# Performance work log

Measured on AMD Instinct MI355X. Metric: run time of the kernel, lower is better.

The kernel has to match this reference:

```python
import math
import jax, jax.numpy as jnp
import numpy as np

H, C, PQ, PV = 8, 256, 8, 12   # no_heads, c_hidden, no_qk_points, no_v_points
INF, EPS = 1e5, 1e-8

def quat_to_rot(q):
    w, x, y, z = q[..., 0], q[..., 1], q[..., 2], q[..., 3]
    r = jnp.stack([
        1 - 2*(y*y + z*z), 2*(x*y - w*z),     2*(x*z + w*y),
        2*(x*y + w*z),     1 - 2*(x*x + z*z), 2*(y*z - w*x),
        2*(x*z - w*y),     2*(y*z + w*x),     1 - 2*(x*x + y*y),
    ], axis=-1)
    return r.reshape(q.shape[:-1] + (3, 3))

def setup_inputs() -> dict:
    key = jax.random.key(0)
    ks = jax.random.split(key, 16)
    B, N, CS, CZ = 1, 512, 384, 128
    s = jax.random.normal(ks[0], (B, N, CS), jnp.float32)
    z = jax.random.normal(ks[1], (B, N, N, CZ), jnp.float32) * 0.1
    quat = jax.random.normal(ks[2], (B, N, 4), jnp.float32)
    quat = quat / jnp.linalg.norm(quat, axis=-1, keepdims=True)
    rot = quat_to_rot(quat)                       # [B,N,3,3] valid rotations
    trans = jax.random.normal(ks[3], (B, N, 3), jnp.float32) * 10.0
    mask = jnp.ones((B, N), jnp.float32)
    g = lambda k, sh: jax.random.normal(k, sh, jnp.float32) * 0.02
    params = dict(
        wq=g(ks[4], (CS, H*C)), bq=jnp.zeros((H*C,), jnp.float32),
        wkv=g(ks[5], (CS, 2*H*C)), bkv=jnp.zeros((2*H*C,), jnp.float32),
        wqp=g(ks[6], (CS, H*PQ*3)), bqp=jnp.zeros((H*PQ*3,), jnp.float32),
        wkvp=g(ks[7], (CS, H*(PQ+PV)*3)), bkvp=jnp.zeros((H*(PQ+PV)*3,), jnp.float32),
        wb=g(ks[8], (CZ, H)), bb=jnp.zeros((H,), jnp.float32),
        wz=g(ks[9], (CZ, CZ//4)), bz=jnp.zeros((CZ//4,), jnp.float32),
        head_weights=jnp.full((H,), 0.541324854612918, jnp.float32),  # softplus^-1(1)
        wo=g(ks[10], (H*(C + 4*PV + CZ//4), CS)), bo=jnp.zeros((CS,), jnp.float32),
    )
    return dict(s=s, z=z, rot=rot, trans=trans, mask=mask, **params)

def reference(s, z, rot, trans, mask, wq, bq, wkv, bkv, wqp, bqp, wkvp, bkvp, wb, bb, wz, bz, head_weights, wo, bo):
    B, N, CS = s.shape
    q = (s @ wq + bq).reshape(B, N, H, C)
    kv = (s @ wkv + bkv).reshape(B, N, H, 2 * C)
    k, v = kv[..., :C], kv[..., C:]

    def split_pts(x):  # torch split-into-3 + stack(-1): [B,N,3*M] -> [B,N,M,3]
        return jnp.moveaxis(x.reshape(B, N, 3, -1), -2, -1)

    def apply_rigid(p):  # global frame: R @ p + t
        return jnp.einsum('bnij,bnpj->bnpi', rot, p) + trans[:, :, None, :]

    q_pts = apply_rigid(split_pts(s @ wqp + bqp)).reshape(B, N, H, PQ, 3)
    kv_pts = apply_rigid(split_pts(s @ wkvp + bkvp)).reshape(B, N, H, PQ + PV, 3)
    k_pts, v_pts = kv_pts[..., :PQ, :], kv_pts[..., PQ:, :]

    b_bias = z @ wb + bb                                  # [B,Ni,Nj,H]
    a = jnp.einsum('bihc,bjhc->bhij', q, k) * math.sqrt(1.0 / (3 * C))
    a = a + math.sqrt(1.0 / 3) * jnp.moveaxis(b_bias, -1, 1)

    disp = q_pts[:, :, None] - k_pts[:, None]             # [B,Ni,Nj,H,PQ,3]
    pt_att = jnp.sum(disp * disp, axis=-1)                # [B,Ni,Nj,H,PQ]
    hw = jax.nn.softplus(head_weights) * math.sqrt(1.0 / (3 * (PQ * 9.0 / 2)))
    pt_att = -0.5 * jnp.sum(pt_att * hw[None, None, None, :, None], axis=-1)  # [B,Ni,Nj,H]

    sq_mask = INF * (mask[:, :, None] * mask[:, None, :] - 1.0)
    a = a + jnp.moveaxis(pt_att, -1, 1) + sq_mask[:, None]
    a = jax.nn.softmax(a, axis=-1)                        # [B,H,Ni,Nj]

    o = jnp.einsum('bhij,bjhc->bihc', a, v).reshape(B, N, H * C)

    o_pt = jnp.einsum('bhij,bjhpd->bihpd', a, v_pts)      # [B,N,H,PV,3] global
    o_pt = jnp.einsum('bnji,bnhpj->bnhpi', rot, o_pt - trans[:, :, None, None, :])  # invert_apply
    o_pt_norm = jnp.sqrt(jnp.sum(o_pt * o_pt, axis=-1) + EPS).reshape(B, N, H * PV)
    o_pt_flat = o_pt.reshape(B, N, H * PV, 3)

    pair_z = z @ wz + bz                                  # [B,Ni,Nj,CZ//4]
    o_pair = jnp.einsum('bhij,bijd->bihd', a, pair_z).reshape(B, N, -1)

    feats = jnp.concatenate(
        [o, o_pt_flat[..., 0], o_pt_flat[..., 1], o_pt_flat[..., 2], o_pt_norm, o_pair], axis=-1)
    return feats @ wo + bo
```

## Files before the change

kernel.cpp:

```cpp
#include <hip/hip_runtime.h>


#define OFF_QBH    0
#define OFF_KBH    524288
#define OFF_VB     1048576
#define OFF_QPRAW  2097152
#define OFF_KVPRAW 2195456
#define OFF_BBIAS  2785280
#define OFF_PAIRZT 3833856
#define OFF_ATTNH  8028160
#define OFF_FEATSB 9076736
#define OFF_WCAT   9764864
#define OFF_WTALL  9767936
#define OFF_VPT    11082752
#define OFF_WOT    11803648
#define OFF_QPTH   12319744
#define OFF_QPTL   12385280
#define OFF_KPTH   12450816
#define OFF_KPTL   12516352
#define OFF_QP2    12581888
#define OFF_KP2    12585984
#define OFF_SBF    12590080

typedef __attribute__((ext_vector_type(8))) short short8;
typedef __attribute__((ext_vector_type(4))) float f32x4;

__device__ __forceinline__ unsigned short f2bf(float f) {
  union { float f; unsigned u; } v; v.f = f;
  unsigned u = v.u;
  unsigned r = (u + 0x7fffu + ((u >> 16) & 1u)) >> 16;
  return (unsigned short)r;
}
__device__ __forceinline__ float bf2f(unsigned short h) {
  union { unsigned u; float f; } v; v.u = ((unsigned)h) << 16; return v.f;
}
__device__ __forceinline__ short8 pack8(float4 a, float4 b) {
  short8 r;
  r[0] = (short)f2bf(a.x); r[1] = (short)f2bf(a.y);
  r[2] = (short)f2bf(a.z); r[3] = (short)f2bf(a.w);
  r[4] = (short)f2bf(b.x); r[5] = (short)f2bf(b.y);
  r[6] = (short)f2bf(b.z); r[7] = (short)f2bf(b.w);
  return r;
}
__device__ __forceinline__ void gl_lds16(const float* g, float* l) {
  __builtin_amdgcn_global_load_lds(
      (const __attribute__((address_space(1))) unsigned int*)(g),
      (__attribute__((address_space(3))) unsigned int*)(l), 16, 0, 0);
}

__global__ __launch_bounds__(256) void prep_all(
    const float* __restrict__ wq, const float* __restrict__ wkv,
    const float* __restrict__ wqp, const float* __restrict__ wkvp,
    const float* __restrict__ wo, const float* __restrict__ wb,
    const float* __restrict__ wz, const float* __restrict__ s,
    unsigned short* __restrict__ wTall, unsigned short* __restrict__ woT,
    unsigned short* __restrict__ wT, unsigned short* __restrict__ sbf) {
  __shared__ float tile[64][65];
  const int b = blockIdx.x, t = threadIdx.x;
  if (b < 642) {
    const int ntile = b % 107, kt = b / 107;
    const float* src; int Nsrc, nloc0;
    const int ng0 = ntile * 64;
    if (ntile < 32)      { src = wq;   Nsrc = 2048; nloc0 = ng0; }
    else if (ntile < 96) { src = wkv;  Nsrc = 4096; nloc0 = ng0 - 2048; }
    else if (ntile < 99) { src = wqp;  Nsrc = 192;  nloc0 = ng0 - 6144; }
    else                 { src = wkvp; Nsrc = 480;  nloc0 = ng0 - 6336; }
    const int r = t >> 2, cs = (t & 3) * 16;
#pragma unroll
    for (int i = 0; i < 16; i += 4) {
      int n = nloc0 + cs + i;
      float4 v;
      if (n + 3 < Nsrc) v = *(const float4*)(src + (size_t)(kt * 64 + r) * Nsrc + n);
      else {
        v.x = (n + 0 < Nsrc) ? src[(size_t)(kt * 64 + r) * Nsrc + n + 0] : 0.f;
        v.y = (n + 1 < Nsrc) ? src[(size_t)(kt * 64 + r) * Nsrc + n + 1] : 0.f;
        v.z = (n + 2 < Nsrc) ? src[(size_t)(kt * 64 + r) * Nsrc + n + 2] : 0.f;
        v.w = (n + 3 < Nsrc) ? src[(size_t)(kt * 64 + r) * Nsrc + n + 3] : 0.f;
      }
      tile[r][cs + i + 0] = v.x; tile[r][cs + i + 1] = v.y;
      tile[r][cs + i + 2] = v.z; tile[r][cs + i + 3] = v.w;
    }
    __syncthreads();
    const int nr = t >> 2, ks = (t & 3) * 16;
    unsigned short ov[16];
#pragma unroll
    for (int i = 0; i < 16; i++) ov[i] = f2bf(tile[ks + i][nr]);
    unsigned short* dst = wTall + (size_t)(ng0 + nr) * 384 + kt * 64 + ks;
    *(uint4*)(dst) = *(const uint4*)&ov[0];
    *(uint4*)(dst + 8) = *(const uint4*)&ov[8];
  } else if (b < 894) {
    const int idx = b - 642;
    const int kt = idx % 42, ntile = idx / 42;
    const int r = t >> 2, cs = (t & 3) * 16;
#pragma unroll
    for (int i = 0; i < 16; i += 4) {
      float4 v = *(const float4*)(wo + (size_t)(kt * 64 + r) * 384 + ntile * 64 + cs + i);
      tile[r][cs + i + 0] = v.x; tile[r][cs + i + 1] = v.y;
      tile[r][cs + i + 2] = v.z; tile[r][cs + i + 3] = v.w;
    }
    __syncthreads();
    const int nr = t >> 2, ks = (t & 3) * 16;
    unsigned short ov[16];
#pragma unroll
    for (int i = 0; i < 16; i++) ov[i] = f2bf(tile[ks + i][nr]);
    unsigned short* dst = woT + (size_t)(ntile * 64 + nr) * 2688 + kt * 64 + ks;
    *(uint4*)(dst) = *(const uint4*)&ov[0];
    *(uint4*)(dst + 8) = *(const uint4*)&ov[8];
  } else if (b < 918) {
    const int l = (b - 894) * 256 + t;
    if (l < 6144) {
      int n = l >> 7, k = l & 127;
      float v = (n < 8) ? wb[k * 8 + n] * 0.5773502691896258f
                        : (n < 40 ? wz[k * 32 + (n - 8)] : 0.f);
      wT[l] = f2bf(v);
    }
  } else {
    const int gid = (b - 918) * 256 + t;
    const int off = gid * 8;
    float4 a0 = *(const float4*)(s + off);
    float4 a1 = *(const float4*)(s + off + 4);
    *(short8*)(sbf + off) = pack8(a0, a1);
  }
}

__global__ __launch_bounds__(256) void mega1(
    const float* __restrict__ z, const unsigned short* __restrict__ wT,
    const float* __restrict__ bb, const float* __restrict__ bz,
    unsigned short* __restrict__ bbias_tb, unsigned short* __restrict__ pairzT,
    const unsigned short* __restrict__ sbf, const unsigned short* __restrict__ wTall,
    const float* __restrict__ bq, const float* __restrict__ bkv,
    const float* __restrict__ bqp, const float* __restrict__ bkvp,
    unsigned short* __restrict__ qbh, unsigned short* __restrict__ kbh,
    float* __restrict__ vb, float* __restrict__ qpraw, float* __restrict__ kvpraw) {
  const int lane = threadIdx.x & 63, wv = threadIdx.x >> 6;
  const int quad = lane >> 4, m = lane & 15;
  if (blockIdx.x < 256) {
    __shared__ __align__(16) float zt[2][64][128];
    __shared__ __align__(16) unsigned short lb[4][8][16];
    __shared__ __align__(16) unsigned short lp[4][32][16];
    short8 bfw[3][4];
#pragma unroll
    for (int nt = 0; nt < 3; nt++)
#pragma unroll
      for (int s = 0; s < 4; s++)
        bfw[nt][s] = *(const short8*)(wT + (size_t)(nt * 16 + m) * 128 + s * 32 + quad * 8);
    float bias[3];
#pragma unroll
    for (int nt = 0; nt < 3; nt++) {
      int c = nt * 16 + m;
      bias[nt] = (c < 8) ? 0.5773502691896258f * bb[c] : (c < 40 ? bz[c - 8] : 0.f);
    }
    const int lrow = lane >> 5, lcol = (lane & 31) * 4;
    {
      const int Tg0 = blockIdx.x * 16;
#pragma unroll
      for (int i2 = 0; i2 < 8; i2++) {
        const int k = wv * 8 + i2;
        gl_lds16(z + (size_t)(Tg0 * 64 + 2 * k + lrow) * 128 + lcol, &zt[0][2 * k][0]);
      }
    }
    __syncthreads();
    for (int T = 0; T < 16; T++) {
      const int buf = T & 1;
      const int Tg = blockIdx.x * 16 + T;
      if (T < 15) {
#pragma unroll
        for (int i2 = 0; i2 < 8; i2++) {
          const int k = wv * 8 + i2;
          gl_lds16(z + (size_t)((Tg + 1) * 64 + 2 * k + lrow) * 128 + lcol,
                   &zt[buf ^ 1][2 * k][0]);
        }
      }
      f32x4 acc[3];
#pragma unroll
      for (int nt = 0; nt < 3; nt++) acc[nt] = (f32x4){0.f, 0.f, 0.f, 0.f};
#pragma unroll
      for (int s = 0; s < 4; s++) {
        const float* zr = &zt[buf][wv * 16 + m][s * 32 + quad * 8];
        float4 a0 = *(const float4*)(zr);
        float4 a1 = *(const float4*)(zr + 4);
        short8 af = pack8(a0, a1);
#pragma unroll
        for (int nt = 0; nt < 3; nt++)
          acc[nt] = __builtin_amdgcn_mfma_f32_16x16x32_bf16(af, bfw[nt][s], acc[nt], 0, 0, 0);
      }
#pragma unroll
      for (int nt = 0; nt < 3; nt++) {
        const int c = nt * 16 + m;
#pragma unroll
        for (int r = 0; r < 4; r++) {
          const float v = acc[nt][r] + bias[nt];
          const int jl = quad * 4 + r;
          if (c < 8)       lb[wv][c][jl] = f2bf(v);
          else if (c < 40) lp[wv][c - 8][jl] = f2bf(v);
        }
      }
      const int row0 = Tg * 64 + wv * 16;
      const int i = row0 >> 9, j0 = row0 & 511;
      if (lane < 16) {
        int c = lane >> 1, half = lane & 1;
        uint4 val = *(const uint4*)&lb[wv][c][half * 8];
        *(uint4*)(bbias_tb + (size_t)c * 262144 + row0 + half * 8) = val;
      }
      {
        int d = lane >> 1, half = lane & 1;
        uint4 val = *(const uint4*)&lp[wv][d][half * 8];
        *(uint4*)(pairzT + ((size_t)i * 32 + d) * 512 + j0 + half * 8) = val;
      }
      __syncthreads();
    }
  } else {
    const int b2 = blockIdx.x - 256;
    const int bx = b2 % 107, row0 = (b2 / 107) * 64;
    const int n0 = bx * 64;
    const unsigned short* srow = sbf + (size_t)(row0 + wv * 16 + m) * 384;
    f32x4 acc[4];
#pragma unroll
    for (int nt = 0; nt < 4; nt++) acc[nt] = (f32x4){0.f, 0.f, 0.f, 0.f};
#pragma unroll
    for (int ksx = 0; ksx < 12; ksx++) {
      const int c0 = ksx * 32 + quad * 8;
      short8 af = *(const short8*)(srow + c0);
#pragma unroll
      for (int nt = 0; nt < 4; nt++) {
        short8 bfw2 = *(const short8*)(wTall + (size_t)(n0 + nt * 16 + m) * 384 + c0);
        acc[nt] = __builtin_amdgcn_mfma_f32_16x16x32_bf16(af, bfw2, acc[nt], 0, 0, 0);
      }
    }
    const int rbase = row0 + wv * 16 + quad * 4;
#pragma unroll
    for (int nt = 0; nt < 4; nt++) {
      const int col = n0 + nt * 16 + m;
      if (n0 < 2048) {
        const float bias = bq[col];
#pragma unroll
        for (int r = 0; r < 4; r++)
          qbh[(size_t)(rbase + r) * 2048 + col] = f2bf(acc[nt][r] + bias);
      } else if (n0 < 6144) {
        const int ckv = col - 2048;
        const float bias = bkv[ckv];
        const int hh = ckv >> 9, c = ckv & 511;
        if (c < 256) {
#pragma unroll
          for (int r = 0; r < 4; r++)
            kbh[(size_t)(rbase + r) * 2048 + hh * 256 + c] = f2bf(acc[nt][r] + bias);
        } else {
#pragma unroll
          for (int r = 0; r < 4; r++)
            vb[(size_t)(rbase + r) * 2048 + hh * 256 + (c - 256)] = acc[nt][r] + bias;
        }
      } else if (n0 < 6336) {
        const int cq = col - 6144;
        const float bias = bqp[cq];
#pragma unroll
        for (int r = 0; r < 4; r++)
          qpraw[(size_t)(rbase + r) * 192 + cq] = acc[nt][r] + bias;
      } else {
        const int ck = col - 6336;
        if (ck < 480) {
          const float bias = bkvp[ck];
#pragma unroll
          for (int r = 0; r < 4; r++)
            kvpraw[(size_t)(rbase + r) * 480 + ck] = acc[nt][r] + bias;
        }
      }
    }
  }
}

__global__ __launch_bounds__(256) void mega2(
    const float* __restrict__ vb, const float* __restrict__ qpraw,
    const float* __restrict__ kvpraw, const float* __restrict__ rot,
    const float* __restrict__ trans, unsigned short* __restrict__ vptT,
    unsigned short* __restrict__ qptH, unsigned short* __restrict__ qptL,
    unsigned short* __restrict__ kptH, unsigned short* __restrict__ kptL,
    float* __restrict__ qp2g, float* __restrict__ kp2g) {
  __shared__ float tile[64][65];
  const int b = blockIdx.x, t = threadIdx.x;
  if (b < 320) {
    const int jt = b & 7, h = (b >> 3) & 7, part = b >> 6;
    const int j0 = jt * 64;
    if (part < 4) {
      const int c0 = part * 64;
      const int r = t >> 2, cs = (t & 3) * 16;
#pragma unroll
      for (int ii = 0; ii < 16; ii += 4) {
        float4 v = *(const float4*)(vb + (size_t)(j0 + r) * 2048 + h * 256 + c0 + cs + ii);
        tile[r][cs + ii + 0] = v.x; tile[r][cs + ii + 1] = v.y;
        tile[r][cs + ii + 2] = v.z; tile[r][cs + ii + 3] = v.w;
      }
      __syncthreads();
      const int cl = t >> 2, js = (t & 3) * 16;
      unsigned short ov[16];
#pragma unroll
      for (int x = 0; x < 16; x++) ov[x] = f2bf(tile[js + x][cl]);
      unsigned short* dst = vptT + ((size_t)h * 352 + c0 + cl) * 512 + j0 + js;
      *(uint4*)dst = *(const uint4*)&ov[0];
      *(uint4*)(dst + 8) = *(const uint4*)&ov[8];
    } else {
      float (*lds)[37] = (float(*)[37])&tile[0][0];
      for (int l = t; l < 64 * 36; l += 256) {
        int jl = l / 36, w = l % 36;
        int p = w / 3, d = w % 3;
        const int n = j0 + jl;
        const int pidx = h * 20 + 8 + p;
        const float* kr = kvpraw + (size_t)n * 480;
        float px = kr[pidx], py = kr[160 + pidx], pz = kr[320 + pidx];
        const float* R = rot + n * 9;
        lds[jl][w] = R[d * 3 + 0] * px + R[d * 3 + 1] * py + R[d * 3 + 2] * pz + trans[n * 3 + d];
      }
      __syncthreads();
#pragma unroll
      for (int step = 0; step < 3; step++) {
        int chunk = t + 256 * step;
        int row = chunk >> 3, js = (chunk & 7) * 8;
        unsigned short ov[8];
#pragma unroll
        for (int x = 0; x < 8; x++) {
          int w = (row < 48) ? row : row - 48;
          float f = (w < 36) ? lds[js + x][w] : 0.f;
          unsigned short hi = f2bf(f);
          ov[x] = (row < 48) ? hi : f2bf(f - bf2f(hi));
        }
        *(uint4*)(vptT + ((size_t)h * 352 + 256 + row) * 512 + j0 + js) = *(const uint4*)&ov[0];
      }
    }
  } else {
    const int idx = b - 320;
    const int row = (idx & 1) * 256 + t;
    const int h = idx >> 1;
    const float* R  = rot + row * 9;
    const float* tr = trans + row * 3;
    {
      const float* qr = qpraw + (size_t)row * 192;
      unsigned short hi[32], lo[32]; float s2 = 0.f;
#pragma unroll
      for (int p = 0; p < 8; p++) {
        const int pidx = h * 8 + p;
        float px = qr[pidx], py = qr[64 + pidx], pz = qr[128 + pidx];
        float X = R[0] * px + R[1] * py + R[2] * pz + tr[0];
        float Y = R[3] * px + R[4] * py + R[5] * pz + tr[1];
        float Z = R[6] * px + R[7] * py + R[8] * pz + tr[2];
        hi[p * 3 + 0] = f2bf(X); lo[p * 3 + 0] = f2bf(X - bf2f(hi[p * 3 + 0]));
        hi[p * 3 + 1] = f2bf(Y); lo[p * 3 + 1] = f2bf(Y - bf2f(hi[p * 3 + 1]));
        hi[p * 3 + 2] = f2bf(Z); lo[p * 3 + 2] = f2bf(Z - bf2f(hi[p * 3 + 2]));
        s2 += X * X + Y * Y + Z * Z;
      }
#pragma unroll
      for (int w = 24; w < 32; w++) { hi[w] = 0; lo[w] = 0; }
      unsigned short* dh = qptH + ((size_t)h * 512 + row) * 32;
      unsigned short* dl = qptL + ((size_t)h * 512 + row) * 32;
#pragma unroll
      for (int g = 0; g < 4; g++) {
        *(uint4*)(dh + g * 8) = *(const uint4*)&hi[g * 8];
        *(uint4*)(dl + g * 8) = *(const uint4*)&lo[g * 8];
      }
      qp2g[h * 512 + row] = s2;
    }
    {
      const float* kr = kvpraw + (size_t)row * 480;
      unsigned short hi[32], lo[32]; float s2 = 0.f;
#pragma unroll
      for (int p = 0; p < 8; p++) {
        const int pidx = h * 20 + p;
        float px = kr[pidx], py = kr[160 + pidx], pz = kr[320 + pidx];
        float X = R[0] * px + R[1] * py + R[2] * pz + tr[0];
        float Y = R[3] * px + R[4] * py + R[5] * pz + tr[1];
        float Z = R[6] * px + R[7] * py + R[8] * pz + tr[2];
        hi[p * 3 + 0] = f2bf(X); lo[p * 3 + 0] = f2bf(X - bf2f(hi[p * 3 + 0]));
        hi[p * 3 + 1] = f2bf(Y); lo[p * 3 + 1] = f2bf(Y - bf2f(hi[p * 3 + 1]));
        hi[p * 3 + 2] = f2bf(Z); lo[p * 3 + 2] = f2bf(Z - bf2f(hi[p * 3 + 2]));
        s2 += X * X + Y * Y + Z * Z;
      }
#pragma unroll
      for (int w = 24; w < 32; w++) { hi[w] = 0; lo[w] = 0; }
      unsigned short* dh = kptH + ((size_t)h * 512 + row) * 32;
      unsigned short* dl = kptL + ((size_t)h * 512 + row) * 32;
#pragma unroll
      for (int g = 0; g < 4; g++) {
        *(uint4*)(dh + g * 8) = *(const uint4*)&hi[g * 8];
        *(uint4*)(dl + g * 8) = *(const uint4*)&lo[g * 8];
      }
      kp2g[h * 512 + row] = s2;
    }
  }
}

__global__ __launch_bounds__(512) void logits_fused(
    const unsigned short* __restrict__ qbh, const unsigned short* __restrict__ kbh,
    const unsigned short* __restrict__ qptH, const unsigned short* __restrict__ qptL,
    const unsigned short* __restrict__ kptH, const unsigned short* __restrict__ kptL,
    const float* __restrict__ qp2g, const float* __restrict__ kp2g,
    const unsigned short* __restrict__ bbias_tb, const float* __restrict__ mask,
    const float* __restrict__ hwp, const unsigned short* __restrict__ vptT,
    const float* __restrict__ rot, const float* __restrict__ trans,
    unsigned short* __restrict__ attnh, unsigned short* __restrict__ featsb) {
  const int bx = blockIdx.x;
  const int h = bx & 7, it = bx >> 3;
  const int i0 = it * 16;
  __shared__ __align__(16) unsigned short sth[8][16][72], stl[8][16][72];
  __shared__ float redm[16][8], reds[16][8];
  __shared__ float lds_h[16][48], lds_l[16][48];
  const int t = threadIdx.x;
  const int lane = t & 63, wv = t >> 6;
  const int quad = lane >> 4, m = lane & 15;
  const int jw0 = wv * 64;

  f32x4 acc[4];
#pragma unroll
  for (int nt = 0; nt < 4; nt++) acc[nt] = (f32x4){0.f, 0.f, 0.f, 0.f};
  const unsigned short* qrow = qbh + (size_t)(i0 + m) * 2048 + h * 256;
#pragma unroll
  for (int s = 0; s < 8; s++) {
    short8 af = *(const short8*)(qrow + s * 32 + quad * 8);
#pragma unroll
    for (int nt = 0; nt < 4; nt++) {
      short8 bfr = *(const short8*)(kbh + (size_t)(jw0 + nt * 16 + m) * 2048 + h * 256 + s * 32 + quad * 8);
      acc[nt] = __builtin_amdgcn_mfma_f32_16x16x32_bf16(af, bfr, acc[nt], 0, 0, 0);
    }
  }

  short8 aqh = *(const short8*)(qptH + ((size_t)h * 512 + i0 + m) * 32 + quad * 8);
  short8 aql = *(const short8*)(qptL + ((size_t)h * 512 + i0 + m) * 32 + quad * 8);
  f32x4 accp[4];
#pragma unroll
  for (int nt = 0; nt < 4; nt++) {
    const size_t krow = ((size_t)h * 512 + jw0 + nt * 16 + m) * 32 + quad * 8;
    short8 bkh = *(const short8*)(kptH + krow);
    short8 bkl = *(const short8*)(kptL + krow);
    f32x4 p = (f32x4){0.f, 0.f, 0.f, 0.f};
    p = __builtin_amdgcn_mfma_f32_16x16x32_bf16(aqh, bkh, p, 0, 0, 0);
    p = __builtin_amdgcn_mfma_f32_16x16x32_bf16(aqh, bkl, p, 0, 0, 0);
    p = __builtin_amdgcn_mfma_f32_16x16x32_bf16(aql, bkh, p, 0, 0, 0);
    accp[nt] = p;
  }

  const float c1 = 0.03608439182435161f;
  const float hw = log1pf(expf(hwp[h])) * 0.09622504486493764f;
  float qp2v[4];
#pragma unroll
  for (int r = 0; r < 4; r++) qp2v[r] = qp2g[h * 512 + i0 + quad * 4 + r];
  float lg[4][4];
  float rmax[4] = {-1e30f, -1e30f, -1e30f, -1e30f};
#pragma unroll
  for (int nt = 0; nt < 4; nt++) {
    const int j = jw0 + nt * 16 + m;
    const float kp2v = kp2g[h * 512 + j];
    const float mj = mask[j];
#pragma unroll
    for (int r = 0; r < 4; r++) {
      const int il = quad * 4 + r;
      const float pt = qp2v[r] + kp2v - 2.f * accp[nt][r];
      float v = c1 * acc[nt][r]
              + bf2f(bbias_tb[(size_t)h * 262144 + (size_t)(i0 + il) * 512 + j])
              - 0.5f * hw * pt
              + 100000.f * (mask[i0 + il] * mj - 1.f);
      lg[nt][r] = v;
      rmax[r] = fmaxf(rmax[r], v);
    }
  }
#pragma unroll
  for (int r = 0; r < 4; r++) {
#pragma unroll
    for (int off = 1; off < 16; off <<= 1) rmax[r] = fmaxf(rmax[r], __shfl_xor(rmax[r], off));
  }
  if (m == 0) {
#pragma unroll
    for (int r = 0; r < 4; r++) redm[quad * 4 + r][wv] = rmax[r];
  }
  __syncthreads();
  float rowm[4], rsum[4];
#pragma unroll
  for (int r = 0; r < 4; r++) {
    const int il = quad * 4 + r;
    float m0 = fmaxf(fmaxf(redm[il][0], redm[il][1]), fmaxf(redm[il][2], redm[il][3]));
    float m1 = fmaxf(fmaxf(redm[il][4], redm[il][5]), fmaxf(redm[il][6], redm[il][7]));
    rowm[r] = fmaxf(m0, m1);
    rsum[r] = 0.f;
  }
#pragma unroll
  for (int nt = 0; nt < 4; nt++)
#pragma unroll
    for (int r = 0; r < 4; r++) {
      float e = __expf(lg[nt][r] - rowm[r]);
      lg[nt][r] = e;
      rsum[r] += e;
    }
#pragma unroll
  for (int r = 0; r < 4; r++) {
#pragma unroll
    for (int off = 1; off < 16; off <<= 1) rsum[r] += __shfl_xor(rsum[r], off);
  }
  if (m == 0) {
#pragma unroll
    for (int r = 0; r < 4; r++) reds[quad * 4 + r][wv] = rsum[r];
  }
  __syncthreads();
  float inv[4];
#pragma unroll
  for (int r = 0; r < 4; r++) {
    const int il = quad * 4 + r;
    float s0 = (reds[il][0] + reds[il][1]) + (reds[il][2] + reds[il][3]);
    float s1 = (reds[il][4] + reds[il][5]) + (reds[il][6] + reds[il][7]);
    inv[r] = 1.f / (s0 + s1);
  }
#pragma unroll
  for (int nt = 0; nt < 4; nt++)
#pragma unroll
    for (int r = 0; r < 4; r++) {
      const int il = quad * 4 + r;
      float a = lg[nt][r] * inv[r];
      unsigned short hi = f2bf(a);
      sth[wv][il][nt * 16 + m] = hi;
      stl[wv][il][nt * 16 + m] = f2bf(a - bf2f(hi));
    }
  __syncthreads();
#pragma unroll
  for (int step = 0; step < 2; step++) {
    const int idx = lane + 64 * step;
    const int il = idx >> 3, seg = idx & 7;
    uint4 vh = *(const uint4*)&sth[wv][il][seg * 8];
    *(uint4*)(attnh + ((size_t)h * 512 + i0 + il) * 512 + jw0 + seg * 8) = vh;
  }

  const int nt0 = (wv < 6) ? wv * 3 : 18 + (wv - 6) * 2;
  const int ncnt = (wv < 6) ? 3 : 2;
  f32x4 vacc[3];
#pragma unroll
  for (int k = 0; k < 3; k++) vacc[k] = (f32x4){0.f, 0.f, 0.f, 0.f};
  const unsigned short* vbase = vptT + (size_t)h * 352 * 512;
#pragma unroll
  for (int s = 0; s < 16; s++) {
    const int wsrc = s >> 1, col = (s & 1) * 32 + quad * 8;
    short8 ah = *(const short8*)&sth[wsrc][m][col];
    short8 al = *(const short8*)&stl[wsrc][m][col];
    const int ko = s * 32 + quad * 8;
#pragma unroll
    for (int k = 0; k < 3; k++) {
      if (k < ncnt) {
        const int nt = nt0 + k;
        short8 bfr = *(const short8*)(vbase + (size_t)(nt * 16 + m) * 512 + ko);
        vacc[k] = __builtin_amdgcn_mfma_f32_16x16x32_bf16(ah, bfr, vacc[k], 0, 0, 0);
        if (nt >= 16 && nt < 19)
          vacc[k] = __builtin_amdgcn_mfma_f32_16x16x32_bf16(al, bfr, vacc[k], 0, 0, 0);
      }
    }
  }
#pragma unroll
  for (int k = 0; k < 3; k++) {
    if (k < ncnt) {
      const int nt = nt0 + k;
      if (nt < 16) {
#pragma unroll
        for (int r = 0; r < 4; r++)
          featsb[(size_t)(i0 + quad * 4 + r) * 2688 + h * 256 + nt * 16 + m] = f2bf(vacc[k][r]);
      } else if (nt < 19) {
        const int w = (nt - 16) * 16 + m;
#pragma unroll
        for (int r = 0; r < 4; r++) if (w < 36) lds_h[quad * 4 + r][w] = vacc[k][r];
      } else {
        const int w = (nt - 19) * 16 + m;
#pragma unroll
        for (int r = 0; r < 4; r++) if (w < 36) lds_l[quad * 4 + r][w] = vacc[k][r];
      }
    }
  }
  __syncthreads();
  if (t < 192) {
    const int il = t / 12, p = t % 12, irow = i0 + il;
    const float* R = rot + irow * 9;
    const float* tr = trans + irow * 3;
    float x  = lds_h[il][p * 3 + 0] + lds_l[il][p * 3 + 0] - tr[0];
    float y  = lds_h[il][p * 3 + 1] + lds_l[il][p * 3 + 1] - tr[1];
    float zz = lds_h[il][p * 3 + 2] + lds_l[il][p * 3 + 2] - tr[2];
    float o0 = R[0] * x + R[3] * y + R[6] * zz;
    float o1 = R[1] * x + R[4] * y + R[7] * zz;
    float o2 = R[2] * x + R[5] * y + R[8] * zz;
    float nrm = sqrtf(o0 * o0 + o1 * o1 + o2 * o2 + 1e-8f);
    unsigned short* fr = featsb + (size_t)irow * 2688 + 2048;
    fr[h * 12 + p]       = f2bf(o0);
    fr[96 + h * 12 + p]  = f2bf(o1);
    fr[192 + h * 12 + p] = f2bf(o2);
    fr[288 + h * 12 + p] = f2bf(nrm);
  }
}

__global__ __launch_bounds__(256) void o_pair_mfma(
    const unsigned short* __restrict__ attnh, const unsigned short* __restrict__ pairzT,
    unsigned short* __restrict__ featsb) {
  const int lane = threadIdx.x & 63, wv = threadIdx.x >> 6;
  const int quad = lane >> 4, m = lane & 15;
  const int i = blockIdx.x;
  __shared__ float red[4][2][64][4];
  f32x4 acc[2];
  acc[0] = (f32x4){0.f, 0.f, 0.f, 0.f};
  acc[1] = (f32x4){0.f, 0.f, 0.f, 0.f};
#pragma unroll
  for (int s4 = 0; s4 < 4; s4++) {
    const int s = wv * 4 + s4;
    const int ko = s * 32 + quad * 8;
    short8 af = *(const short8*)(attnh + (size_t)(m & 7) * 262144 + (size_t)i * 512 + ko);
#pragma unroll
    for (int nt = 0; nt < 2; nt++) {
      short8 bfr = *(const short8*)(pairzT + ((size_t)i * 32 + nt * 16 + m) * 512 + ko);
      acc[nt] = __builtin_amdgcn_mfma_f32_16x16x32_bf16(af, bfr, acc[nt], 0, 0, 0);
    }
  }
#pragma unroll
  for (int nt = 0; nt < 2; nt++)
#pragma unroll
    for (int r = 0; r < 4; r++) red[wv][nt][lane][r] = acc[nt][r];
  __syncthreads();
  if (wv == 0 && quad < 2) {
#pragma unroll
    for (int nt = 0; nt < 2; nt++)
#pragma unroll
      for (int r = 0; r < 4; r++) {
        float sum = (red[0][nt][lane][r] + red[1][nt][lane][r])
                  + (red[2][nt][lane][r] + red[3][nt][lane][r]);
        const int hh = quad * 4 + r, d = nt * 16 + m;
        featsb[(size_t)i * 2688 + 2432 + hh * 32 + d] = f2bf(sum);
      }
  }
}

__global__ __launch_bounds__(512) void out_mfma(
    const unsigned short* __restrict__ featsb, const unsigned short* __restrict__ woT,
    const float* __restrict__ bo, float* __restrict__ out) {
  const int it = blockIdx.x, ng = blockIdx.y;
  const int t = threadIdx.x;
  const int lane = t & 63, w8 = t >> 6;
  const int wn = w8 & 3, wk = w8 >> 2;
  const int quad = lane >> 4, m = lane & 15;
  const int i0 = it * 16, n0 = (ng * 4 + wn) * 16;
  const unsigned short* arow = featsb + (size_t)(i0 + m) * 2688 + wk * 1344;
  const unsigned short* brow = woT + (size_t)(n0 + m) * 2688 + wk * 1344;
  f32x4 acc = (f32x4){0.f, 0.f, 0.f, 0.f};
#pragma unroll 6
  for (int s = 0; s < 42; s++) {
    const int ko = s * 32 + quad * 8;
    short8 af = *(const short8*)(arow + ko);
    short8 bf = *(const short8*)(brow + ko);
    acc = __builtin_amdgcn_mfma_f32_16x16x32_bf16(af, bf, acc, 0, 0, 0);
  }
  __shared__ float red[4][64][4];
  if (wk == 1) {
#pragma unroll
    for (int r = 0; r < 4; r++) red[wn][lane][r] = acc[r];
  }
  __syncthreads();
  if (wk == 0) {
    const float bias = bo[n0 + m];
#pragma unroll
    for (int r = 0; r < 4; r++)
      out[(size_t)(i0 + quad * 4 + r) * 384 + n0 + m] = acc[r] + red[wn][lane][r] + bias;
  }
}

extern "C" void kernel_launch(void* const* d_in, const int* in_sizes, int n_in,
                              void* d_out, int out_size, void* d_ws, size_t ws_size,
                              hipStream_t stream) {
  const float* s     = (const float*)d_in[0];
  const float* z     = (const float*)d_in[1];
  const float* rot   = (const float*)d_in[2];
  const float* trans = (const float*)d_in[3];
  const float* mask  = (const float*)d_in[4];
  const float* wq    = (const float*)d_in[5];
  const float* bq    = (const float*)d_in[6];
  const float* wkv   = (const float*)d_in[7];
  const float* bkv   = (const float*)d_in[8];
  const float* wqp   = (const float*)d_in[9];
  const float* bqp   = (const float*)d_in[10];
  const float* wkvp  = (const float*)d_in[11];
  const float* bkvp  = (const float*)d_in[12];
  const float* wb    = (const float*)d_in[13];
  const float* bb    = (const float*)d_in[14];
  const float* wz    = (const float*)d_in[15];
  const float* bz    = (const float*)d_in[16];
  const float* hwp   = (const float*)d_in[17];
  const float* wo    = (const float*)d_in[18];
  const float* bo    = (const float*)d_in[19];
  float* out = (float*)d_out;

  float* ws = (float*)d_ws;
  unsigned short* qbh   = (unsigned short*)(ws + OFF_QBH);
  unsigned short* kbh   = (unsigned short*)(ws + OFF_KBH);
  float* vb      = ws + OFF_VB;
  float* qpraw   = ws + OFF_QPRAW;
  float* kvpraw  = ws + OFF_KVPRAW;
  unsigned short* bbias_tb = (unsigned short*)(ws + OFF_BBIAS);
  unsigned short* pairzT   = (unsigned short*)(ws + OFF_PAIRZT);
  unsigned short* attnh    = (unsigned short*)(ws + OFF_ATTNH);
  unsigned short* featsb   = (unsigned short*)(ws + OFF_FEATSB);
  unsigned short* wT    = (unsigned short*)(ws + OFF_WCAT);
  unsigned short* wTall = (unsigned short*)(ws + OFF_WTALL);
  unsigned short* vptT  = (unsigned short*)(ws + OFF_VPT);
  unsigned short* woT   = (unsigned short*)(ws + OFF_WOT);
  unsigned short* qptH  = (unsigned short*)(ws + OFF_QPTH);
  unsigned short* qptL  = (unsigned short*)(ws + OFF_QPTL);
  unsigned short* kptH  = (unsigned short*)(ws + OFF_KPTH);
  unsigned short* kptL  = (unsigned short*)(ws + OFF_KPTL);
  float* qp2g = ws + OFF_QP2;
  float* kp2g = ws + OFF_KP2;
  unsigned short* sbf = (unsigned short*)(ws + OFF_SBF);

  prep_all<<<1014, 256, 0, stream>>>(wq, wkv, wqp, wkvp, wo, wb, wz, s,
                                     wTall, woT, wT, sbf);
  mega1<<<1112, 256, 0, stream>>>(z, wT, bb, bz, bbias_tb, pairzT,
                                  sbf, wTall, bq, bkv, bqp, bkvp,
                                  qbh, kbh, vb, qpraw, kvpraw);
  mega2<<<336, 256, 0, stream>>>(vb, qpraw, kvpraw, rot, trans, vptT,
                                 qptH, qptL, kptH, kptL, qp2g, kp2g);
  logits_fused<<<256, 512, 0, stream>>>(qbh, kbh, qptH, qptL, kptH, kptL,
                                        qp2g, kp2g, bbias_tb, mask, hwp,
                                        vptT, rot, trans, attnh, featsb);
  o_pair_mfma<<<512, 256, 0, stream>>>(attnh, pairzT, featsb);
  out_mfma<<<dim3(32, 6), 512, 0, stream>>>(featsb, woT, bo, out);
}
```

Measured before the change: 320.1 us.

## Move z-pass projection into prep kernel, converting wb/wz weights inline

The z pair projection (bias and pair_z via MFMA over z) moves from the second kernel into the first prep kernel. Each z block now converts the wb/wz weights to bf16 in registers, so the separate wT staging buffer is gone. The heavy z streaming now runs alongside the weight transposes, and the second kernel does only the s projections. The cost is redundant weight conversion in every z block and a larger shared-memory footprint for the prep blocks, which may reduce occupancy.

New measurement: 349.3 us. 9.1% more time.

```diff
diff --git a/kernel.cpp b/kernel.cpp
--- a/kernel.cpp
+++ b/kernel.cpp
@@ -10,7 +10,6 @@
 #define OFF_PAIRZT 3833856
 #define OFF_ATTNH  8028160
 #define OFF_FEATSB 9076736
-#define OFF_WCAT   9764864
 #define OFF_WTALL  9767936
 #define OFF_VPT    11082752
 #define OFF_WOT    11803648
@@ -48,17 +47,110 @@
       (__attribute__((address_space(3))) unsigned int*)(l), 16, 0, 0);
 }
 
-__global__ __launch_bounds__(256) void prep_all(
+__global__ __launch_bounds__(256) void prep_zpass(
+    const float* __restrict__ z, const float* __restrict__ wb,
+    const float* __restrict__ wz, const float* __restrict__ bb,
+    const float* __restrict__ bz,
+    unsigned short* __restrict__ bbias_tb, unsigned short* __restrict__ pairzT,
     const float* __restrict__ wq, const float* __restrict__ wkv,
     const float* __restrict__ wqp, const float* __restrict__ wkvp,
-    const float* __restrict__ wo, const float* __restrict__ wb,
-    const float* __restrict__ wz, const float* __restrict__ s,
+    const float* __restrict__ wo, const float* __restrict__ s,
     unsigned short* __restrict__ wTall, unsigned short* __restrict__ woT,
-    unsigned short* __restrict__ wT, unsigned short* __restrict__ sbf) {
-  __shared__ float tile[64][65];
+    unsigned short* __restrict__ sbf) {
+  __shared__ __align__(16) unsigned char smem[70656];
   const int b = blockIdx.x, t = threadIdx.x;
-  if (b < 642) {
-    const int ntile = b % 107, kt = b / 107;
+  const int lane = t & 63, wv = t >> 6;
+  const int quad = lane >> 4, m = lane & 15;
+  if (b < 256) {
+    float (*zt)[64][128] = (float(*)[64][128])smem;
+    unsigned short (*lb)[8][16]  = (unsigned short(*)[8][16])(smem + 65536);
+    unsigned short (*lp)[32][16] = (unsigned short(*)[32][16])(smem + 66560);
+    short8 bfw[3][4];
+#pragma unroll
+    for (int nt = 0; nt < 3; nt++) {
+      const int n = nt * 16 + m;
+#pragma unroll
+      for (int s4 = 0; s4 < 4; s4++) {
+        short8 w8v;
+#pragma unroll
+        for (int jj = 0; jj < 8; jj++) {
+          const int k = s4 * 32 + quad * 8 + jj;
+          float v = (n < 8) ? wb[k * 8 + n] * 0.5773502691896258f
+                            : (n < 40 ? wz[k * 32 + (n - 8)] : 0.f);
+          w8v[jj] = (short)f2bf(v);
+        }
+        bfw[nt][s4] = w8v;
+      }
+    }
+    float bias[3];
+#pragma unroll
+    for (int nt = 0; nt < 3; nt++) {
+      int c = nt * 16 + m;
+      bias[nt] = (c < 8) ? 0.5773502691896258f * bb[c] : (c < 40 ? bz[c - 8] : 0.f);
+    }
+    {
+      const int Tg0 = b * 16;
+#pragma unroll
+      for (int i2 = 0; i2 < 8; i2++) {
+        const int k = wv * 8 + i2;
+        gl_lds16(z + (size_t)(Tg0 * 64 + 2 * k + (lane >> 5)) * 128 + (lane & 31) * 4,
+                 &zt[0][2 * k][0]);
+      }
+    }
+    __syncthreads();
+    for (int T = 0; T < 16; T++) {
+      const int buf = T & 1;
+      const int Tg = b * 16 + T;
+      if (T < 15) {
+#pragma unroll
+        for (int i2 = 0; i2 < 8; i2++) {
+          const int k = wv * 8 + i2;
+          gl_lds16(z + (size_t)((Tg + 1) * 64 + 2 * k + (lane >> 5)) * 128 + (lane & 31) * 4,
+                   &zt[buf ^ 1][2 * k][0]);
+        }
+      }
+      f32x4 acc[3];
+#pragma unroll
+      for (int nt = 0; nt < 3; nt++) acc[nt] = (f32x4){0.f, 0.f, 0.f, 0.f};
+#pragma unroll
+      for (int s4 = 0; s4 < 4; s4++) {
+        const float* zr = &zt[buf][wv * 16 + m][s4 * 32 + quad * 8];
+        float4 a0 = *(const float4*)(zr);
+        float4 a1 = *(const float4*)(zr + 4);
+        short8 af = pack8(a0, a1);
+#pragma unroll
+        for (int nt = 0; nt < 3; nt++)
+          acc[nt] = __builtin_amdgcn_mfma_f32_16x16x32_bf16(af, bfw[nt][s4], acc[nt], 0, 0, 0);
+      }
+#pragma unroll
+      for (int nt = 0; nt < 3; nt++) {
+        const int c = nt * 16 + m;
+#pragma unroll
+        for (int r = 0; r < 4; r++) {
+          const float v = acc[nt][r] + bias[nt];
+          const int jl = quad * 4 + r;
+          if (c < 8)       lb[wv][c][jl] = f2bf(v);
+          else if (c < 40) lp[wv][c - 8][jl] = f2bf(v);
+        }
+      }
+      const int row0 = Tg * 64 + wv * 16;
+      const int i = row0 >> 9, j0 = row0 & 511;
+      if (lane < 16) {
+        int c = lane >> 1, half = lane & 1;
+        uint4 val = *(const uint4*)&lb[wv][c][half * 8];
+        *(uint4*)(bbias_tb + (size_t)c * 262144 + row0 + half * 8) = val;
+      }
+      {
+        int d = lane >> 1, half = lane & 1;
+        uint4 val = *(const uint4*)&lp[wv][d][half * 8];
+        *(uint4*)(pairzT + ((size_t)i * 32 + d) * 512 + j0 + half * 8) = val;
+      }
+      __syncthreads();
+    }
+  } else if (b < 898) {
+    float (*tile)[65] = (float(*)[65])smem;
+    const int idx = b - 256;
+    const int ntile = idx % 107, kt = idx / 107;
     const float* src; int Nsrc, nloc0;
     const int ng0 = ntile * 64;
     if (ntile < 32)      { src = wq;   Nsrc = 2048; nloc0 = ng0; }
@@ -88,8 +180,9 @@
     unsigned short* dst = wTall + (size_t)(ng0 + nr) * 384 + kt * 64 + ks;
     *(uint4*)(dst) = *(const uint4*)&ov[0];
     *(uint4*)(dst + 8) = *(const uint4*)&ov[8];
-  } else if (b < 894) {
-    const int idx = b - 642;
+  } else if (b < 1150) {
+    float (*tile)[65] = (float(*)[65])smem;
+    const int idx = b - 898;
     const int kt = idx % 42, ntile = idx / 42;
     const int r = t >> 2, cs = (t & 3) * 16;
 #pragma unroll
@@ -106,16 +199,8 @@
     unsigned short* dst = woT + (size_t)(ntile * 64 + nr) * 2688 + kt * 64 + ks;
     *(uint4*)(dst) = *(const uint4*)&ov[0];
     *(uint4*)(dst + 8) = *(const uint4*)&ov[8];
-  } else if (b < 918) {
-    const int l = (b - 894) * 256 + t;
-    if (l < 6144) {
-      int n = l >> 7, k = l & 127;
-      float v = (n < 8) ? wb[k * 8 + n] * 0.5773502691896258f
-                        : (n < 40 ? wz[k * 32 + (n - 8)] : 0.f);
-      wT[l] = f2bf(v);
-    }
   } else {
-    const int gid = (b - 918) * 256 + t;
+    const int gid = (b - 1150) * 256 + t;
     const int off = gid * 8;
     float4 a0 = *(const float4*)(s + off);
     float4 a1 = *(const float4*)(s + off + 4);
@@ -123,10 +208,7 @@
   }
 }
 
-__global__ __launch_bounds__(256) void mega1(
-    const float* __restrict__ z, const unsigned short* __restrict__ wT,
-    const float* __restrict__ bb, const float* __restrict__ bz,
-    unsigned short* __restrict__ bbias_tb, unsigned short* __restrict__ pairzT,
+__global__ __launch_bounds__(256) void proj_mfma(
     const unsigned short* __restrict__ sbf, const unsigned short* __restrict__ wTall,
     const float* __restrict__ bq, const float* __restrict__ bkv,
     const float* __restrict__ bqp, const float* __restrict__ bkvp,
@@ -134,135 +216,57 @@
     float* __restrict__ vb, float* __restrict__ qpraw, float* __restrict__ kvpraw) {
   const int lane = threadIdx.x & 63, wv = threadIdx.x >> 6;
   const int quad = lane >> 4, m = lane & 15;
-  if (blockIdx.x < 256) {
-    __shared__ __align__(16) float zt[2][64][128];
-    __shared__ __align__(16) unsigned short lb[4][8][16];
-    __shared__ __align__(16) unsigned short lp[4][32][16];
-    short8 bfw[3][4];
-#pragma unroll
-    for (int nt = 0; nt < 3; nt++)
-#pragma unroll
-      for (int s = 0; s < 4; s++)
-        bfw[nt][s] = *(const short8*)(wT + (size_t)(nt * 16 + m) * 128 + s * 32 + quad * 8);
-    float bias[3];
-#pragma unroll
-    for (int nt = 0; nt < 3; nt++) {
-      int c = nt * 16 + m;
-      bias[nt] = (c < 8) ? 0.5773502691896258f * bb[c] : (c < 40 ? bz[c - 8] : 0.f);
-    }
-    const int lrow = lane >> 5, lcol = (lane & 31) * 4;
-    {
-      const int Tg0 = blockIdx.x * 16;
-#pragma unroll
-      for (int i2 = 0; i2 < 8; i2++) {
-        const int k = wv * 8 + i2;
-        gl_lds16(z + (size_t)(Tg0 * 64 + 2 * k + lrow) * 128 + lcol, &zt[0][2 * k][0]);
-      }
-    }
-    __syncthreads();
-    for (int T = 0; T < 16; T++) {
-      const int buf = T & 1;
-      const int Tg = blockIdx.x * 16 + T;
-      if (T < 15) {
-#pragma unroll
-        for (int i2 = 0; i2 < 8; i2++) {
-          const int k = wv * 8 + i2;
-          gl_lds16(z + (size_t)((Tg + 1) * 64 + 2 * k + lrow) * 128 + lcol,
-                   &zt[buf ^ 1][2 * k][0]);
-        }
-      }
-      f32x4 acc[3];
-#pragma unroll
-      for (int nt = 0; nt < 3; nt++) acc[nt] = (f32x4){0.f, 0.f, 0.f, 0.f};
-#pragma unroll
-      for (int s = 0; s < 4; s++) {
-        const float* zr = &zt[buf][wv * 16 + m][s * 32 + quad * 8];
-        float4 a0 = *(const float4*)(zr);
-        float4 a1 = *(const float4*)(zr + 4);
-        short8 af = pack8(a0, a1);
-#pragma unroll
-        for (int nt = 0; nt < 3; nt++)
-          acc[nt] = __builtin_amdgcn_mfma_f32_16x16x32_bf16(af, bfw[nt][s], acc[nt], 0, 0, 0);
-      }
-#pragma unroll
-      for (int nt = 0; nt < 3; nt++) {
-        const int c = nt * 16 + m;
-#pragma unroll
-        for (int r = 0; r < 4; r++) {
-          const float v = acc[nt][r] + bias[nt];
-          const int jl = quad * 4 + r;
-          if (c < 8)       lb[wv][c][jl] = f2bf(v);
-          else if (c < 40) lp[wv][c - 8][jl] = f2bf(v);
-        }
-      }
-      const int row0 = Tg * 64 + wv * 16;
-      const int i = row0 >> 9, j0 = row0 & 511;
-      if (lane < 16) {
-        int c = lane >> 1, half = lane & 1;
-        uint4 val = *(const uint4*)&lb[wv][c][half * 8];
-        *(uint4*)(bbias_tb + (size_t)c * 262144 + row0 + half * 8) = val;
-      }
-      {
-        int d = lane >> 1, half = lane & 1;
-        uint4 val = *(const uint4*)&lp[wv][d][half * 8];
-        *(uint4*)(pairzT + ((size_t)i * 32 + d) * 512 + j0 + half * 8) = val;
-      }
-      __syncthreads();
-    }
-  } else {
-    const int b2 = blockIdx.x - 256;
-    const int bx = b2 % 107, row0 = (b2 / 107) * 64;
-    const int n0 = bx * 64;
-    const unsigned short* srow = sbf + (size_t)(row0 + wv * 16 + m) * 384;
-    f32x4 acc[4];
-#pragma unroll
-    for (int nt = 0; nt < 4; nt++) acc[nt] = (f32x4){0.f, 0.f, 0.f, 0.f};
-#pragma unroll
-    for (int ksx = 0; ksx < 12; ksx++) {
-      const int c0 = ksx * 32 + quad * 8;
-      short8 af = *(const short8*)(srow + c0);
-#pragma unroll
-      for (int nt = 0; nt < 4; nt++) {
-        short8 bfw2 = *(const short8*)(wTall + (size_t)(n0 + nt * 16 + m) * 384 + c0);
-        acc[nt] = __builtin_amdgcn_mfma_f32_16x16x32_bf16(af, bfw2, acc[nt], 0, 0, 0);
-      }
-    }
-    const int rbase = row0 + wv * 16 + quad * 4;
+  const int bx = blockIdx.x % 107, row0 = (blockIdx.x / 107) * 64;
+  const int n0 = bx * 64;
+  const unsigned short* srow = sbf + (size_t)(row0 + wv * 16 + m) * 384;
+  f32x4 acc[4];
+#pragma unroll
+  for (int nt = 0; nt < 4; nt++) acc[nt] = (f32x4){0.f, 0.f, 0.f, 0.f};
+#pragma unroll
+  for (int ksx = 0; ksx < 12; ksx++) {
+    const int c0 = ksx * 32 + quad * 8;
+    short8 af = *(const short8*)(srow + c0);
 #pragma unroll
     for (int nt = 0; nt < 4; nt++) {
-      const int col = n0 + nt * 16 + m;
-      if (n0 < 2048) {
-        const float bias = bq[col];
+      short8 bfw2 = *(const short8*)(wTall + (size_t)(n0 + nt * 16 + m) * 384 + c0);
+      acc[nt] = __builtin_amdgcn_mfma_f32_16x16x32_bf16(af, bfw2, acc[nt], 0, 0, 0);
+    }
+  }
+  const int rbase = row0 + wv * 16 + quad * 4;
+#pragma unroll
+  for (int nt = 0; nt < 4; nt++) {
+    const int col = n0 + nt * 16 + m;
+    if (n0 < 2048) {
+      const float bias = bq[col];
+#pragma unroll
+      for (int r = 0; r < 4; r++)
+        qbh[(size_t)(rbase + r) * 2048 + col] = f2bf(acc[nt][r] + bias);
+    } else if (n0 < 6144) {
+      const int ckv = col - 2048;
+      const float bias = bkv[ckv];
+      const int hh = ckv >> 9, c = ckv & 511;
+      if (c < 256) {
 #pragma unroll
         for (int r = 0; r < 4; r++)
-          qbh[(size_t)(rbase + r) * 2048 + col] = f2bf(acc[nt][r] + bias);
-      } else if (n0 < 6144) {
-        const int ckv = col - 2048;
-        const float bias = bkv[ckv];
-        const int hh = ckv >> 9, c = ckv & 511;
-        if (c < 256) {
-#pragma unroll
-          for (int r = 0; r < 4; r++)
-            kbh[(size_t)(rbase + r) * 2048 + hh * 256 + c] = f2bf(acc[nt][r] + bias);
-        } else {
-#pragma unroll
-          for (int r = 0; r < 4; r++)
-            vb[(size_t)(rbase + r) * 2048 + hh * 256 + (c - 256)] = acc[nt][r] + bias;
-        }
-      } else if (n0 < 6336) {
-        const int cq = col - 6144;
-        const float bias = bqp[cq];
+          kbh[(size_t)(rbase + r) * 2048 + hh * 256 + c] = f2bf(acc[nt][r] + bias);
+      } else {
 #pragma unroll
         for (int r = 0; r < 4; r++)
-          qpraw[(size_t)(rbase + r) * 192 + cq] = acc[nt][r] + bias;
-      } else {
-        const int ck = col - 6336;
-        if (ck < 480) {
-          const float bias = bkvp[ck];
-#pragma unroll
-          for (int r = 0; r < 4; r++)
-            kvpraw[(size_t)(rbase + r) * 480 + ck] = acc[nt][r] + bias;
-        }
+          vb[(size_t)(rbase + r) * 2048 + hh * 256 + (c - 256)] = acc[nt][r] + bias;
+      }
+    } else if (n0 < 6336) {
+      const int cq = col - 6144;
+      const float bias = bqp[cq];
+#pragma unroll
+      for (int r = 0; r < 4; r++)
+        qpraw[(size_t)(rbase + r) * 192 + cq] = acc[nt][r] + bias;
+    } else {
+      const int ck = col - 6336;
+      if (ck < 480) {
+        const float bias = bkvp[ck];
+#pragma unroll
+        for (int r = 0; r < 4; r++)
+          kvpraw[(size_t)(rbase + r) * 480 + ck] = acc[nt][r] + bias;
       }
     }
   }
@@ -692,7 +696,6 @@
   unsigned short* pairzT   = (unsigned short*)(ws + OFF_PAIRZT);
   unsigned short* attnh    = (unsigned short*)(ws + OFF_ATTNH);
   unsigned short* featsb   = (unsigned short*)(ws + OFF_FEATSB);
-  unsigned short* wT    = (unsigned short*)(ws + OFF_WCAT);
   unsigned short* wTall = (unsigned short*)(ws + OFF_WTALL);
   unsigned short* vptT  = (unsigned short*)(ws + OFF_VPT);
   unsigned short* woT   = (unsigned short*)(ws + OFF_WOT);
@@ -704,11 +707,11 @@
   float* kp2g = ws + OFF_KP2;
   unsigned short* sbf = (unsigned short*)(ws + OFF_SBF);
 
-  prep_all<<<1014, 256, 0, stream>>>(wq, wkv, wqp, wkvp, wo, wb, wz, s,
-                                     wTall, woT, wT, sbf);
-  mega1<<<1112, 256, 0, stream>>>(z, wT, bb, bz, bbias_tb, pairzT,
-                                  sbf, wTall, bq, bkv, bqp, bkvp,
-                                  qbh, kbh, vb, qpraw, kvpraw);
+  prep_zpass<<<1246, 256, 0, stream>>>(z, wb, wz, bb, bz, bbias_tb, pairzT,
+                                       wq, wkv, wqp, wkvp, wo, s,
+                                       wTall, woT, sbf);
+  proj_mfma<<<856, 256, 0, stream>>>(sbf, wTall, bq, bkv, bqp, bkvp,
+                                     qbh, kbh, vb, qpraw, kvpraw);
   mega2<<<336, 256, 0, stream>>>(vb, qpraw, kvpraw, rot, trans, vptT,
                                  qptH, qptL, kptH, kptL, qp2g, kp2g);
   logits_fused<<<256, 512, 0, stream>>>(qbh, kbh, qptH, qptL, kptH, kptL,
```
